# Kernel tuning notes

Measured on AMD Instinct MI355X. Metric: run time of the kernel, lower is better.

Reference implementation:

```python
import jax, jax.numpy as jnp
import numpy as np

R, C, N, E, H, F, ED, G, L = 1, 4, 50000, 200000, 128, 128, 16, 64, 2


def setup_inputs() -> dict:
    key = jax.random.key(0)
    ks = jax.random.split(key, 16)
    s = 0.05
    return {
        "x": jax.random.normal(ks[0], (R * C * N, H), jnp.float32),
        "batch": jnp.sort(jax.random.randint(ks[1], (N,), 0, G)),
        "edge_index": jax.random.randint(ks[2], (2, E), 0, N),
        "edge_attr": jax.random.normal(ks[3], (1, 1, E, ED), jnp.float32),
        "node_mask": jax.random.uniform(ks[4], (R, C, N, 1), jnp.float32),
        "edge_mask": jax.random.uniform(ks[5], (R, C, E, 1), jnp.float32),
        "W_be": jax.random.normal(ks[6], (ED, H), jnp.float32) * s,
        "b_be": jnp.zeros((H,), jnp.float32),
        "eps": jnp.zeros((L,), jnp.float32),
        "W1": jax.random.normal(ks[7], (L, H, H), jnp.float32) * s,
        "b1": jnp.zeros((L, H), jnp.float32),
        "W2": jax.random.normal(ks[8], (L, H, H), jnp.float32) * s,
        "b2": jnp.zeros((L, H), jnp.float32),
        "Wm1": jax.random.normal(ks[9], (H, H), jnp.float32) * s,
        "bm1": jnp.zeros((H,), jnp.float32),
        "Wm2": jax.random.normal(ks[10], (H, F), jnp.float32) * s,
        "bm2": jnp.zeros((F,), jnp.float32),
    }


def reference(x, batch, edge_index, edge_attr, node_mask, edge_mask,
              W_be, b_be, eps, W1, b1, W2, b2, Wm1, bm1, Wm2, bm2):
    gelu = lambda v: jax.nn.gelu(v, approximate=False)  # torch F.gelu default is erf
    src, dst = edge_index[0], edge_index[1]
    # bond encoder, shared across conv layers: (1,1,E,H)
    ee = edge_attr @ W_be + b_be
    for l in range(L):
        ux = x.reshape(R, C, N, H)
        # gather + add + GELU + edge-weight multiply: (R,C,E,H)
        msg = gelu(ux[:, :, src, :] + ee) * edge_mask
        # scatter_sum over edges into destination nodes
        agg = jnp.zeros_like(ux).at[:, :, dst, :].add(msg)
        h = (1.0 + eps[l]) * x + agg.reshape(x.shape)
        # conv MLP: Linear -> GELU -> Linear, then outer GELU (norm=Identity, dropout=0)
        h = gelu(h @ W1[l] + b1[l]) @ W2[l] + b2[l]
        x = gelu(h)
    # final node MLP (PyG MLP, norm=None): Linear -> GELU -> Linear
    x = gelu(x @ Wm1 + bm1) @ Wm2 + bm2  # (R*C*N, F)
    x4 = x.reshape(R, C, N, F)
    # masked mean-pool per (repeat, centroid, graph)
    num = jnp.zeros((R, C, G, F), x.dtype).at[:, :, batch, :].add(x4 * node_mask)
    den = jnp.zeros((R, C, G, 1), x.dtype).at[:, :, batch, :].add(node_mask) + 1e-7
    pooled = (num / den).transpose(0, 2, 1, 3).reshape(-1, F)  # (R*G*C, F)
    return pooled
```

## Files before the change

### kernel.cpp

```cpp
#include <hip/hip_runtime.h>
#include <math.h>

#define NN 50000
#define EN 200000
#define CC 4
#define HH 128
#define GG 64
#define LDSA 136
#define LDSF 132

typedef __attribute__((ext_vector_type(8))) short bs8;
typedef __attribute__((ext_vector_type(4))) float f32x4;
typedef __attribute__((ext_vector_type(2))) float f32x2;

__device__ __forceinline__ unsigned short f2bf(float f) {
  unsigned int u = __float_as_uint(f);
  u += 0x7FFFu + ((u >> 16) & 1u);
  return (unsigned short)(u >> 16);
}
__device__ __forceinline__ float bf2f(unsigned short h) {
  return __uint_as_float(((unsigned int)h) << 16);
}
__device__ __forceinline__ float gelu_f(float x) {
  float z = fabsf(x) * 0.7071067811865476f;
  float t = __builtin_amdgcn_rcpf(fmaf(0.3275911f, z, 1.0f));
  float poly = t * fmaf(t, fmaf(t, fmaf(t, fmaf(t, 1.061405429f, -1.453152027f),
                                        1.421413741f), -0.284496736f), 0.254829592f);
  float e = fmaf(-poly, __expf(-z * z), 1.0f);
  return 0.5f * x * (1.0f + copysignf(e, x));
}
__device__ __forceinline__ float gelu2_f(float x) {
  float z = fabsf(x) * 0.7071067811865476f;
  float t = __builtin_amdgcn_rcpf(fmaf(0.3275911f, z, 1.0f));
  float poly = t * fmaf(t, fmaf(t, fmaf(t, fmaf(t, 1.061405429f, -1.453152027f),
                                        1.421413741f), -0.284496736f), 0.254829592f);
  float e = fmaf(-poly, __expf(-z * z), 1.0f);
  return x * (1.0f + copysignf(e, x));
}

__global__ __launch_bounds__(256) void count_kernel(const int* __restrict__ dst,
                                                    int* __restrict__ counts) {
  int e = blockIdx.x * 256 + threadIdx.x;
  if (e < EN) atomicAdd(&counts[dst[e]], 1);
}

__global__ __launch_bounds__(256) void block_sum_kernel(const int* __restrict__ counts,
                                                        int* __restrict__ bsums) {
  int tid = threadIdx.x;
  int i = blockIdx.x * 256 + tid;
  int v = (i < NN) ? counts[i] : 0;
#pragma unroll
  for (int d = 1; d < 64; d <<= 1) v += __shfl_xor(v, d);
  __shared__ int ws4[4];
  if ((tid & 63) == 0) ws4[tid >> 6] = v;
  __syncthreads();
  if (tid == 0) bsums[blockIdx.x] = ws4[0] + ws4[1] + ws4[2] + ws4[3];
}

__global__ __launch_bounds__(256) void bsum_scan_kernel(const int* __restrict__ bsums,
                                                        int* __restrict__ boffs, int nb) {
  int tid = threadIdx.x, lane = tid & 63, wv = tid >> 6;
  int v = (tid < nb) ? bsums[tid] : 0;
  int s = v;
#pragma unroll
  for (int d = 1; d < 64; d <<= 1) { int t = __shfl_up(s, d); if (lane >= d) s += t; }
  __shared__ int wsum[4];
  if (lane == 63) wsum[wv] = s;
  __syncthreads();
  int pre = 0;
  for (int j = 0; j < wv; ++j) pre += wsum[j];
  if (tid < nb) boffs[tid] = pre + s - v;
}

__global__ __launch_bounds__(256) void block_scan_kernel(const int* __restrict__ counts,
// ... 41 lines not shown
                                                     unsigned short* __restrict__ wts) {
  int m = blockIdx.x >> 6;
  int idx = (blockIdx.x & 63) * 256 + threadIdx.x;
  const float* src = (m == 0) ? W1 : (m == 1) ? W1 + 16384 : (m == 2) ? W2
                     : (m == 3) ? W2 + 16384 : (m == 4) ? Wm1 : Wm2;
  unsigned short* dhi = wts + m * 32768;
  unsigned short* dlo = dhi + 16384;
  int n = idx >> 7, k = idx & 127;
  float v = src[k * HH + n];
  unsigned short hi = f2bf(v);
  dhi[n * HH + k] = hi;
  dlo[n * HH + k] = f2bf(v - bf2f(hi));
}

__global__ __launch_bounds__(256) void ee_kernel(const float* __restrict__ eattr,
                                                 const float* __restrict__ Wbe,
                                                 const float* __restrict__ bbe,
                                                 float* __restrict__ ee) {
  __shared__ float Ws[16 * HH];
  __shared__ float Ea[16 * 16];
  int tid = threadIdx.x;
  int e0 = blockIdx.x * 16;
#pragma unroll
  for (int i = 0; i < 8; ++i) Ws[tid + i * 256] = Wbe[tid + i * 256];
  Ea[tid] = eattr[(size_t)e0 * 16 + tid];
  __syncthreads();
  int h = tid & 127, half = tid >> 7;
  float bb = bbe[h];
#pragma unroll
  for (int j = 0; j < 8; ++j) {
    int el = j * 2 + half;
    float acc = bb;
#pragma unroll
    for (int d = 0; d < 16; ++d) acc += Ea[el * 16 + d] * Ws[d * HH + h];
    ee[(size_t)(e0 + el) * HH + h] = acc;
  }
}

__global__ __launch_bounds__(256) void agg_kernel(const float* __restrict__ x,
                                                  const float* __restrict__ ee,
                                                  const int* __restrict__ off,
                                                  const int2* __restrict__ csr_es,
                                                  const float4* __restrict__ emask_s,
                                                  const float* __restrict__ epsp, int layer,
                                                  float* __restrict__ hout) {
  int wv = threadIdx.x >> 6, lane = threadIdx.x & 63;
  int v = blockIdx.x * 4 + wv;
  int c2 = lane * 2;
  float2 acc[CC];
#pragma unroll
  for (int c = 0; c < CC; ++c) { acc[c].x = 0.f; acc[c].y = 0.f; }
  int beg = off[v], end = off[v + 1];

  float2 eeC; float2 xC[CC]; float emC[CC];
  int2 esN = make_int2(0, 0);
  eeC.x = 0.f; eeC.y = 0.f;
#pragma unroll
  for (int c = 0; c < CC; ++c) { xC[c].x = 0.f; xC[c].y = 0.f; emC[c] = 0.f; }

  if (beg < end) {
    int2 es0 = csr_es[beg];
    eeC = *(const float2*)(ee + (size_t)es0.x * HH + c2);
#pragma unroll
    for (int c = 0; c < CC; ++c)
      xC[c] = *(const float2*)(x + ((size_t)c * NN + es0.y) * HH + c2);
    float4 m = emask_s[beg];
    emC[0] = 0.5f * m.x; emC[1] = 0.5f * m.y; emC[2] = 0.5f * m.z; emC[3] = 0.5f * m.w;
    if (beg + 1 < end) esN = csr_es[beg + 1];
  }

  for (int t = beg; t < end; ++t) {
    float2 eeB; float2 xB[CC]; float emB[CC];
    int2 esNN = make_int2(0, 0);
    if (t + 1 < end) {
      eeB = *(const float2*)(ee + (size_t)esN.x * HH + c2);
#pragma unroll
      for (int c = 0; c < CC; ++c)
        xB[c] = *(const float2*)(x + ((size_t)c * NN + esN.y) * HH + c2);
      float4 m = emask_s[t + 1];
      emB[0] = 0.5f * m.x; emB[1] = 0.5f * m.y; emB[2] = 0.5f * m.z; emB[3] = 0.5f * m.w;
      if (t + 2 < end) esNN = csr_es[t + 2];
    } else {
      eeB.x = 0.f; eeB.y = 0.f;
#pragma unroll
      for (int c = 0; c < CC; ++c) { xB[c].x = 0.f; xB[c].y = 0.f; emB[c] = 0.f; }
    }
#pragma unroll
    for (int c = 0; c < CC; ++c) {
      acc[c].x += gelu2_f(xC[c].x + eeC.x) * emC[c];
      acc[c].y += gelu2_f(xC[c].y + eeC.y) * emC[c];
    }
    eeC = eeB;
#pragma unroll
    for (int c = 0; c < CC; ++c) { xC[c] = xB[c]; emC[c] = emB[c]; }
    esN = esNN;
  }

  float ep = 1.0f + epsp[layer];
#pragma unroll
  for (int c = 0; c < CC; ++c) {
    float2 xs = *(const float2*)(x + ((size_t)c * NN + v) * HH + c2);
    f32x2 o;
    o[0] = fmaf(ep, xs.x, acc[c].x);
    o[1] = fmaf(ep, xs.y, acc[c].y);
    __builtin_nontemporal_store(o, (f32x2*)(hout + ((size_t)c * NN + v) * HH + c2));
  }
}

__global__ __launch_bounds__(256, 2) void mlp_kernel(
    const float* __restrict__ in,
    const unsigned short* __restrict__ w1hi, const unsigned short* __restrict__ w1lo,
    const float* __restrict__ b1,
    const unsigned short* __restrict__ w2hi, const unsigned short* __restrict__ w2lo,
    const float* __restrict__ b2,
    float* __restrict__ out) {
  __shared__ __align__(16) unsigned short AB[2 * 64 * HH];
  unsigned short* Ahi = AB;
  unsigned short* Alo = AB + 64 * HH;
  int tid = threadIdx.x;
  int row0 = blockIdx.x * 64;
  int lane = tid & 63, wq = tid >> 6;
  int ln = lane & 15, quad = lane >> 4;

  bs8 b1h[4][2], b1l[4][2];
#pragma unroll
  for (int ks = 0; ks < 4; ++ks)
#pragma unroll
    for (int nt = 0; nt < 2; ++nt) {
      int wrow = ((wq * 2 + nt) * 16 + ln) * HH + ks * 32 + quad * 8;
      b1h[ks][nt] = *(const bs8*)(w1hi + wrow);
      b1l[ks][nt] = *(const bs8*)(w1lo + wrow);
    }

#pragma unroll
  for (int i = 0; i < 4; ++i) {
    int idx = tid + i * 256;
    int r = idx >> 4, blk = idx & 15;
    const float* p = in + (size_t)(row0 + r) * HH + blk * 8;
    f32x4 v0 = __builtin_nontemporal_load((const f32x4*)p);
    f32x4 v1 = __builtin_nontemporal_load((const f32x4*)(p + 4));
    bs8 h, l;
    h[0] = f2bf(v0[0]); h[1] = f2bf(v0[1]); h[2] = f2bf(v0[2]); h[3] = f2bf(v0[3]);
    h[4] = f2bf(v1[0]); h[5] = f2bf(v1[1]); h[6] = f2bf(v1[2]); h[7] = f2bf(v1[3]);
    l[0] = f2bf(v0[0] - bf2f(h[0])); l[1] = f2bf(v0[1] - bf2f(h[1]));
    l[2] = f2bf(v0[2] - bf2f(h[2])); l[3] = f2bf(v0[3] - bf2f(h[3]));
    l[4] = f2bf(v1[0] - bf2f(h[4])); l[5] = f2bf(v1[1] - bf2f(h[5]));
    l[6] = f2bf(v1[2] - bf2f(h[6])); l[7] = f2bf(v1[3] - bf2f(h[7]));
    int sb = blk ^ (r & 15);
    *(bs8*)(Ahi + r * HH + sb * 8) = h;
    *(bs8*)(Alo + r * HH + sb * 8) = l;
  }
  __syncthreads();

  f32x4 acc[4][2];
#pragma unroll
  for (int mt = 0; mt < 4; ++mt)
#pragma unroll
    for (int nt = 0; nt < 2; ++nt)
#pragma unroll
      for (int r = 0; r < 4; ++r) acc[mt][nt][r] = 0.f;
#pragma unroll
  for (int ks = 0; ks < 4; ++ks) {
    bs8 ah[4], al[4];
    int sb = ((ks * 4 + quad) ^ ln) * 8;
#pragma unroll
    for (int mt = 0; mt < 4; ++mt) {
      ah[mt] = *(const bs8*)(Ahi + (mt * 16 + ln) * HH + sb);
      al[mt] = *(const bs8*)(Alo + (mt * 16 + ln) * HH + sb);
    }
#pragma unroll
    for (int nt = 0; nt < 2; ++nt)
#pragma unroll
      for (int mt = 0; mt < 4; ++mt) {
        acc[mt][nt] = __builtin_amdgcn_mfma_f32_16x16x32_bf16(al[mt], b1h[ks][nt], acc[mt][nt], 0, 0, 0);
        acc[mt][nt] = __builtin_amdgcn_mfma_f32_16x16x32_bf16(ah[mt], b1l[ks][nt], acc[mt][nt], 0, 0, 0);
        acc[mt][nt] = __builtin_amdgcn_mfma_f32_16x16x32_bf16(ah[mt], b1h[ks][nt], acc[mt][nt], 0, 0, 0);
      }
  }
  __syncthreads();

  bs8 b2h[4][2], b2l[4][2];
#pragma unroll
  for (int ks = 0; ks < 4; ++ks)
#pragma unroll
    for (int nt = 0; nt < 2; ++nt) {
      int wrow = ((wq * 2 + nt) * 16 + ln) * HH + ks * 32 + quad * 8;
      b2h[ks][nt] = *(const bs8*)(w2hi + wrow);
      b2l[ks][nt] = *(const bs8*)(w2lo + wrow);
    }

#pragma unroll
  for (int nt = 0; nt < 2; ++nt) {
    int col = (wq * 2 + nt) * 16 + ln;
    int cb = col >> 3, co = col & 7;
    float bb = b1[col];
#pragma unroll
    for (int mt = 0; mt < 4; ++mt)
#pragma unroll
      for (int r = 0; r < 4; ++r) {
        float tv = gelu_f(acc[mt][nt][r] + bb);
        unsigned short th = f2bf(tv);
        int rr = mt * 16 + quad * 4 + r;
        int sof = rr * HH + (cb ^ (rr & 15)) * 8 + co;
        Ahi[sof] = th;
        Alo[sof] = f2bf(tv - bf2f(th));
      }
  }
  __syncthreads();

#pragma unroll
  for (int mt = 0; mt < 4; ++mt)
#pragma unroll
    for (int nt = 0; nt < 2; ++nt)
#pragma unroll
      for (int r = 0; r < 4; ++r) acc[mt][nt][r] = 0.f;
#pragma unroll
  for (int ks = 0; ks < 4; ++ks) {
    bs8 ah[4], al[4];
    int sb = ((ks * 4 + quad) ^ ln) * 8;
#pragma unroll
    for (int mt = 0; mt < 4; ++mt) {
      ah[mt] = *(const bs8*)(Ahi + (mt * 16 + ln) * HH + sb);
      al[mt] = *(const bs8*)(Alo + (mt * 16 + ln) * HH + sb);
    }
#pragma unroll
    for (int nt = 0; nt < 2; ++nt)
#pragma unroll
      for (int mt = 0; mt < 4; ++mt) {
        acc[mt][nt] = __builtin_amdgcn_mfma_f32_16x16x32_bf16(al[mt], b2h[ks][nt], acc[mt][nt], 0, 0, 0);
        acc[mt][nt] = __builtin_amdgcn_mfma_f32_16x16x32_bf16(ah[mt], b2l[ks][nt], acc[mt][nt], 0, 0, 0);
        acc[mt][nt] = __builtin_amdgcn_mfma_f32_16x16x32_bf16(ah[mt], b2h[ks][nt], acc[mt][nt], 0, 0, 0);
      }
  }
#pragma unroll
  for (int nt = 0; nt < 2; ++nt) {
    int col = (wq * 2 + nt) * 16 + ln;
    float bb = b2[col];
#pragma unroll
    for (int mt = 0; mt < 4; ++mt)
#pragma unroll
      for (int r = 0; r < 4; ++r) {
        float o = gelu_f(acc[mt][nt][r] + bb);
        out[(size_t)(row0 + mt * 16 + quad * 4 + r) * HH + col] = o;
      }
  }
}

__global__ __launch_bounds__(256, 2) void mlp_pool_kernel(
    const float* __restrict__ in,
    const unsigned short* __restrict__ w1hi, const unsigned short* __restrict__ w1lo,
    const float* __restrict__ b1,
    const unsigned short* __restrict__ w2hi, const unsigned short* __restrict__ w2lo,
    const float* __restrict__ b2,
    const float* __restrict__ nmask, const int* __restrict__ batch,
    float* __restrict__ num) {
  __shared__ __align__(16) unsigned short AB[128 * LDSA];
  __shared__ int kk[64];
  unsigned short* Ahi = AB;
  unsigned short* Alo = AB + 64 * LDSA;
  int tid = threadIdx.x;
  int row0 = blockIdx.x * 64;
  int lane = tid & 63, wq = tid >> 6;
  int ln = lane & 15, quad = lane >> 4;

  bs8 b1h[4][2], b1l[4][2];
#pragma unroll
  for (int ks = 0; ks < 4; ++ks)
#pragma unroll
    for (int nt = 0; nt < 2; ++nt) {
      int wrow = ((wq * 2 + nt) * 16 + ln) * HH + ks * 32 + quad * 8;
      b1h[ks][nt] = *(const bs8*)(w1hi + wrow);
      b1l[ks][nt] = *(const bs8*)(w1lo + wrow);
    }
#pragma unroll
  for (int i = 0; i < 8; ++i) {
    int idx = tid + i * 256;
    int r = idx >> 5, cc4 = idx & 31;
    f32x4 vv = __builtin_nontemporal_load(
        (const f32x4*)(in + (size_t)(row0 + r) * HH + cc4 * 4));
    unsigned short h0 = f2bf(vv[0]), h1 = f2bf(vv[1]), h2 = f2bf(vv[2]), h3 = f2bf(vv[3]);
    ushort4 hv; hv.x = h0; hv.y = h1; hv.z = h2; hv.w = h3;
    ushort4 lv;
    lv.x = f2bf(vv[0] - bf2f(h0)); lv.y = f2bf(vv[1] - bf2f(h1));
    lv.z = f2bf(vv[2] - bf2f(h2)); lv.w = f2bf(vv[3] - bf2f(h3));
    *(ushort4*)(Ahi + r * LDSA + cc4 * 4) = hv;
    *(ushort4*)(Alo + r * LDSA + cc4 * 4) = lv;
  }
  if (tid < 64) {
    int gr = row0 + tid;
    int c = gr / NN;
    int n = gr - c * NN;
    kk[tid] = (c << 6) | batch[n];
  }
  __syncthreads();

  f32x4 acc[4][2];
#pragma unroll
  for (int mt = 0; mt < 4; ++mt)
#pragma unroll
    for (int nt = 0; nt < 2; ++nt)
#pragma unroll
      for (int r = 0; r < 4; ++r) acc[mt][nt][r] = 0.f;
#pragma unroll
  for (int ks = 0; ks < 4; ++ks) {
    bs8 ah[4], al[4];
#pragma unroll
    for (int mt = 0; mt < 4; ++mt) {
      ah[mt] = *(const bs8*)(Ahi + (mt * 16 + ln) * LDSA + ks * 32 + quad * 8);
      al[mt] = *(const bs8*)(Alo + (mt * 16 + ln) * LDSA + ks * 32 + quad * 8);
    }
#pragma unroll
    for (int nt = 0; nt < 2; ++nt)
#pragma unroll
      for (int mt = 0; mt < 4; ++mt) {
        acc[mt][nt] = __builtin_amdgcn_mfma_f32_16x16x32_bf16(al[mt], b1h[ks][nt], acc[mt][nt], 0, 0, 0);
        acc[mt][nt] = __builtin_amdgcn_mfma_f32_16x16x32_bf16(ah[mt], b1l[ks][nt], acc[mt][nt], 0, 0, 0);
        acc[mt][nt] = __builtin_amdgcn_mfma_f32_16x16x32_bf16(ah[mt], b1h[ks][nt], acc[mt][nt], 0, 0, 0);
      }
  }
  __syncthreads();

  bs8 b2h[4][2], b2l[4][2];
#pragma unroll
  for (int ks = 0; ks < 4; ++ks)
#pragma unroll
    for (int nt = 0; nt < 2; ++nt) {
      int wrow = ((wq * 2 + nt) * 16 + ln) * HH + ks * 32 + quad * 8;
      b2h[ks][nt] = *(const bs8*)(w2hi + wrow);
      b2l[ks][nt] = *(const bs8*)(w2lo + wrow);
    }
#pragma unroll
  for (int nt = 0; nt < 2; ++nt) {
    int col = (wq * 2 + nt) * 16 + ln;
    float bb = b1[col];
#pragma unroll
    for (int mt = 0; mt < 4; ++mt)
#pragma unroll
      for (int r = 0; r < 4; ++r) {
        float tv = gelu_f(acc[mt][nt][r] + bb);
        unsigned short th = f2bf(tv);
        int rr = mt * 16 + quad * 4 + r;
        Ahi[rr * LDSA + col] = th;
        Alo[rr * LDSA + col] = f2bf(tv - bf2f(th));
      }
  }
  __syncthreads();

#pragma unroll
  for (int mt = 0; mt < 4; ++mt)
#pragma unroll
    for (int nt = 0; nt < 2; ++nt)
#pragma unroll
      for (int r = 0; r < 4; ++r) acc[mt][nt][r] = 0.f;
#pragma unroll
  for (int ks = 0; ks < 4; ++ks) {
    bs8 ah[4], al[4];
#pragma unroll
    for (int mt = 0; mt < 4; ++mt) {
      ah[mt] = *(const bs8*)(Ahi + (mt * 16 + ln) * LDSA + ks * 32 + quad * 8);
      al[mt] = *(const bs8*)(Alo + (mt * 16 + ln) * LDSA + ks * 32 + quad * 8);
    }
#pragma unroll
    for (int nt = 0; nt < 2; ++nt)
#pragma unroll
      for (int mt = 0; mt < 4; ++mt) {
        acc[mt][nt] = __builtin_amdgcn_mfma_f32_16x16x32_bf16(al[mt], b2h[ks][nt], acc[mt][nt], 0, 0, 0);
        acc[mt][nt] = __builtin_amdgcn_mfma_f32_16x16x32_bf16(ah[mt], b2l[ks][nt], acc[mt][nt], 0, 0, 0);
        acc[mt][nt] = __builtin_amdgcn_mfma_f32_16x16x32_bf16(ah[mt], b2h[ks][nt], acc[mt][nt], 0, 0, 0);
      }
  }
  __syncthreads();
  float* Tf = (float*)AB;
#pragma unroll
  for (int nt = 0; nt < 2; ++nt) {
    int col = (wq * 2 + nt) * 16 + ln;
    float bb = b2[col];
#pragma unroll
    for (int mt = 0; mt < 4; ++mt)
#pragma unroll
      for (int r = 0; r < 4; ++r) {
        int rl = mt * 16 + quad * 4 + r;
        int gr = row0 + rl;
        Tf[rl * LDSF + col] = (acc[mt][nt][r] + bb) * nmask[gr];
      }
  }
  __syncthreads();
  if (tid < 128) {
    int col = tid;
    float a2 = 0.f;
    int cur = kk[0];
    for (int r = 0; r < 64; ++r) {
      int k2 = kk[r];
      if (k2 != cur) {
        atomicAdd(&num[((size_t)(cur & 63) * CC + (cur >> 6)) * HH + col], a2);
        a2 = 0.f;
        cur = k2;
      }
      a2 += Tf[r * LDSF + col];
    }
    atomicAdd(&num[((size_t)(cur & 63) * CC + (cur >> 6)) * HH + col], a2);
  }
}

__global__ __launch_bounds__(256) void pool_finalize_kernel(const float* __restrict__ num,
                                                            const int* __restrict__ batch,
                                                            const float* __restrict__ nmask,
                                                            float* __restrict__ outp) {
  int g = blockIdx.x >> 2, c = blockIdx.x & 3;
  int lo = 0, hi = NN;
  while (lo < hi) { int m = (lo + hi) >> 1; if (batch[m] < g) lo = m + 1; else hi = m; }
  int start = lo;
  hi = NN;
  while (lo < hi) { int m = (lo + hi) >> 1; if (batch[m] < g + 1) lo = m + 1; else hi = m; }
  int end = lo;
  int tid = threadIdx.x;
  float d = 0.f;
  for (int n = start + tid; n < end; n += 256) d += nmask[c * NN + n];
#pragma unroll
  for (int k = 1; k < 64; k <<= 1) d += __shfl_xor(d, k);
  __shared__ float ws4[4];
  if ((tid & 63) == 0) ws4[tid >> 6] = d;
// ... 8 lines not shown
extern "C" void kernel_launch(void* const* d_in, const int* in_sizes, int n_in,
                              void* d_out, int out_size, void* d_ws, size_t ws_size,
                              hipStream_t stream) {
  const float* x_in  = (const float*)d_in[0];
  const int*   batch = (const int*)d_in[1];
  const int*   eidx  = (const int*)d_in[2];
  const float* eattr = (const float*)d_in[3];
  const float* nmask = (const float*)d_in[4];
  const float* emask = (const float*)d_in[5];
  const float* Wbe   = (const float*)d_in[6];
  const float* bbe   = (const float*)d_in[7];
  const float* epsp  = (const float*)d_in[8];
  const float* W1    = (const float*)d_in[9];
  const float* b1    = (const float*)d_in[10];
  const float* W2    = (const float*)d_in[11];
  const float* b2    = (const float*)d_in[12];
  const float* Wm1   = (const float*)d_in[13];
  const float* bm1   = (const float*)d_in[14];
  const float* Wm2   = (const float*)d_in[15];
  const float* bm2   = (const float*)d_in[16];
  float* outp = (float*)d_out;

  const int* srcp = eidx;
  const int* dstp = eidx + EN;

  char* ws = (char*)d_ws;
  float* ee   = (float*)(ws);
  float* hbuf = (float*)(ws + 102400000);
  float* xbuf = (float*)(ws + 204800000);
  int* counts  = (int*)(ws + 307200000);
  int* offsets = (int*)(ws + 307400000);
  int* cursor  = (int*)(ws + 307600008);
  int2* csr_es = (int2*)(ws + 307800016);
  float4* emask_s = (float4*)(ws + 309400016);
  unsigned short* wts = (unsigned short*)(ws + 312600016);
  int* bsums = (int*)ws;
  int* boffs = (int*)(ws + 1024);
  float* num = (float*)ws;

  const int NB = (NN + 255) / 256;

  hipMemsetAsync(counts, 0, NN * sizeof(int), stream);
  count_kernel<<<(EN + 255) / 256, 256, 0, stream>>>(dstp, counts);
  block_sum_kernel<<<NB, 256, 0, stream>>>(counts, bsums);
  bsum_scan_kernel<<<1, 256, 0, stream>>>(bsums, boffs, NB);
  block_scan_kernel<<<NB, 256, 0, stream>>>(counts, boffs, offsets, cursor);
  fill_kernel<<<(EN + 255) / 256, 256, 0, stream>>>(dstp, srcp, emask, cursor, csr_es, emask_s);

  prep_w_kernel<<<384, 256, 0, stream>>>(W1, W2, Wm1, Wm2, wts);

  ee_kernel<<<EN / 16, 256, 0, stream>>>(eattr, Wbe, bbe, ee);

  agg_kernel<<<NN / 4, 256, 0, stream>>>(x_in, ee, offsets, csr_es, emask_s, epsp, 0, hbuf);
  mlp_kernel<<<(CC * NN) / 64, 256, 0, stream>>>(hbuf, wts + 0, wts + 16384, b1,
                                                 wts + 65536, wts + 81920, b2, xbuf);
  agg_kernel<<<NN / 4, 256, 0, stream>>>(xbuf, ee, offsets, csr_es, emask_s, epsp, 1, hbuf);
  mlp_kernel<<<(CC * NN) / 64, 256, 0, stream>>>(hbuf, wts + 32768, wts + 49152, b1 + 128,
                                                 wts + 98304, wts + 114688, b2 + 128, xbuf);
  hipMemsetAsync(num, 0, 131072, stream);
  mlp_pool_kernel<<<(CC * NN) / 64, 256, 0, stream>>>(xbuf, wts + 131072, wts + 147456, bm1,
                                                      wts + 163840, wts + 180224, bm2,
                                                      nmask, batch, num);
  pool_finalize_kernel<<<GG * CC, 256, 0, stream>>>(num, batch, nmask, outp);
}
```

Before: 717.2 us.

## Load MLP input fragments directly from global and stream weights per k-step

The first GEMM of both MLP kernels now loads its A fragments straight from global memory into registers, converting to bf16 hi/lo there instead of staging through LDS, and drops one barrier. Weight fragments are loaded per k-step instead of being held for all k-steps, and launch bounds rise from 2 to 4 blocks per CU. The aim is to cut register pressure and LDS traffic so occupancy goes up and latency is hidden better. In exchange, every wave now reads the same input rows from global memory, giving 4x redundant (mostly cached) loads and weight reloads inside the k loop.

```diff
diff --git a/kernel.cpp b/kernel.cpp
--- a/kernel.cpp
+++ b/kernel.cpp
@@ -20,6 +20,14 @@
 }
 __device__ __forceinline__ float bf2f(unsigned short h) {
   return __uint_as_float(((unsigned int)h) << 16);
+}
+__device__ __forceinline__ void cvt_hi_lo(const f32x4& v0, const f32x4& v1, bs8& h, bs8& l) {
+  h[0] = f2bf(v0[0]); h[1] = f2bf(v0[1]); h[2] = f2bf(v0[2]); h[3] = f2bf(v0[3]);
+  h[4] = f2bf(v1[0]); h[5] = f2bf(v1[1]); h[6] = f2bf(v1[2]); h[7] = f2bf(v1[3]);
+  l[0] = f2bf(v0[0] - bf2f(h[0])); l[1] = f2bf(v0[1] - bf2f(h[1]));
+  l[2] = f2bf(v0[2] - bf2f(h[2])); l[3] = f2bf(v0[3] - bf2f(h[3]));
+  l[4] = f2bf(v1[0] - bf2f(h[4])); l[5] = f2bf(v1[1] - bf2f(h[5]));
+  l[6] = f2bf(v1[2] - bf2f(h[6])); l[7] = f2bf(v1[3] - bf2f(h[7]));
 }
 __device__ __forceinline__ float gelu_f(float x) {
   float z = fabsf(x) * 0.7071067811865476f;
@@ -222,7 +230,7 @@
   }
 }
 
-__global__ __launch_bounds__(256, 2) void mlp_kernel(
+__global__ __launch_bounds__(256, 4) void mlp_kernel(
     const float* __restrict__ in,
     const unsigned short* __restrict__ w1hi, const unsigned short* __restrict__ w1lo,
     const float* __restrict__ b1,
@@ -237,72 +245,38 @@
   int lane = tid & 63, wq = tid >> 6;
   int ln = lane & 15, quad = lane >> 4;
 
-  bs8 b1h[4][2], b1l[4][2];
-#pragma unroll
-  for (int ks = 0; ks < 4; ++ks)
+  f32x4 acc[4][2];
+#pragma unroll
+  for (int mt = 0; mt < 4; ++mt)
+#pragma unroll
+    for (int nt = 0; nt < 2; ++nt)
+#pragma unroll
+      for (int r = 0; r < 4; ++r) acc[mt][nt][r] = 0.f;
+
+#pragma unroll
+  for (int ks = 0; ks < 4; ++ks) {
+    bs8 bh[2], bl[2];
 #pragma unroll
     for (int nt = 0; nt < 2; ++nt) {
       int wrow = ((wq * 2 + nt) * 16 + ln) * HH + ks * 32 + quad * 8;
-      b1h[ks][nt] = *(const bs8*)(w1hi + wrow);
-      b1l[ks][nt] = *(const bs8*)(w1lo + wrow);
-    }
-
-#pragma unroll
-  for (int i = 0; i < 4; ++i) {
-    int idx = tid + i * 256;
-    int r = idx >> 4, blk = idx & 15;
-    const float* p = in + (size_t)(row0 + r) * HH + blk * 8;
-    f32x4 v0 = __builtin_nontemporal_load((const f32x4*)p);
-    f32x4 v1 = __builtin_nontemporal_load((const f32x4*)(p + 4));
-    bs8 h, l;
-    h[0] = f2bf(v0[0]); h[1] = f2bf(v0[1]); h[2] = f2bf(v0[2]); h[3] = f2bf(v0[3]);
-    h[4] = f2bf(v1[0]); h[5] = f2bf(v1[1]); h[6] = f2bf(v1[2]); h[7] = f2bf(v1[3]);
-    l[0] = f2bf(v0[0] - bf2f(h[0])); l[1] = f2bf(v0[1] - bf2f(h[1]));
-    l[2] = f2bf(v0[2] - bf2f(h[2])); l[3] = f2bf(v0[3] - bf2f(h[3]));
-    l[4] = f2bf(v1[0] - bf2f(h[4])); l[5] = f2bf(v1[1] - bf2f(h[5]));
-    l[6] = f2bf(v1[2] - bf2f(h[6])); l[7] = f2bf(v1[3] - bf2f(h[7]));
-    int sb = blk ^ (r & 15);
-    *(bs8*)(Ahi + r * HH + sb * 8) = h;
-    *(bs8*)(Alo + r * HH + sb * 8) = l;
-  }
-  __syncthreads();
-
-  f32x4 acc[4][2];
-#pragma unroll
-  for (int mt = 0; mt < 4; ++mt)
-#pragma unroll
-    for (int nt = 0; nt < 2; ++nt)
-#pragma unroll
-      for (int r = 0; r < 4; ++r) acc[mt][nt][r] = 0.f;
-#pragma unroll
-  for (int ks = 0; ks < 4; ++ks) {
-    bs8 ah[4], al[4];
-    int sb = ((ks * 4 + quad) ^ ln) * 8;
+      bh[nt] = *(const bs8*)(w1hi + wrow);
+      bl[nt] = *(const bs8*)(w1lo + wrow);
+    }
 #pragma unroll
     for (int mt = 0; mt < 4; ++mt) {
-      ah[mt] = *(const bs8*)(Ahi + (mt * 16 + ln) * HH + sb);
-      al[mt] = *(const bs8*)(Alo + (mt * 16 + ln) * HH + sb);
-    }
-#pragma unroll
-    for (int nt = 0; nt < 2; ++nt)
-#pragma unroll
-      for (int mt = 0; mt < 4; ++mt) {
-        acc[mt][nt] = __builtin_amdgcn_mfma_f32_16x16x32_bf16(al[mt], b1h[ks][nt], acc[mt][nt], 0, 0, 0);
-        acc[mt][nt] = __builtin_amdgcn_mfma_f32_16x16x32_bf16(ah[mt], b1l[ks][nt], acc[mt][nt], 0, 0, 0);
-        acc[mt][nt] = __builtin_amdgcn_mfma_f32_16x16x32_bf16(ah[mt], b1h[ks][nt], acc[mt][nt], 0, 0, 0);
-      }
-  }
-  __syncthreads();
-
-  bs8 b2h[4][2], b2l[4][2];
-#pragma unroll
-  for (int ks = 0; ks < 4; ++ks)
-#pragma unroll
-    for (int nt = 0; nt < 2; ++nt) {
-      int wrow = ((wq * 2 + nt) * 16 + ln) * HH + ks * 32 + quad * 8;
-      b2h[ks][nt] = *(const bs8*)(w2hi + wrow);
-      b2l[ks][nt] = *(const bs8*)(w2lo + wrow);
-    }
+      const float* p = in + (size_t)(row0 + mt * 16 + ln) * HH + ks * 32 + quad * 8;
+      f32x4 v0 = __builtin_nontemporal_load((const f32x4*)p);
+      f32x4 v1 = __builtin_nontemporal_load((const f32x4*)(p + 4));
+      bs8 ah, al;
+      cvt_hi_lo(v0, v1, ah, al);
+#pragma unroll
+      for (int nt = 0; nt < 2; ++nt) {
+        acc[mt][nt] = __builtin_amdgcn_mfma_f32_16x16x32_bf16(al, bh[nt], acc[mt][nt], 0, 0, 0);
+        acc[mt][nt] = __builtin_amdgcn_mfma_f32_16x16x32_bf16(ah, bl[nt], acc[mt][nt], 0, 0, 0);
+        acc[mt][nt] = __builtin_amdgcn_mfma_f32_16x16x32_bf16(ah, bh[nt], acc[mt][nt], 0, 0, 0);
+      }
+    }
+  }
 
 #pragma unroll
   for (int nt = 0; nt < 2; ++nt) {
@@ -331,6 +305,13 @@
       for (int r = 0; r < 4; ++r) acc[mt][nt][r] = 0.f;
 #pragma unroll
   for (int ks = 0; ks < 4; ++ks) {
+    bs8 bh[2], bl[2];
+#pragma unroll
+    for (int nt = 0; nt < 2; ++nt) {
+      int wrow = ((wq * 2 + nt) * 16 + ln) * HH + ks * 32 + quad * 8;
+      bh[nt] = *(const bs8*)(w2hi + wrow);
+      bl[nt] = *(const bs8*)(w2lo + wrow);
+    }
     bs8 ah[4], al[4];
     int sb = ((ks * 4 + quad) ^ ln) * 8;
 #pragma unroll
@@ -339,12 +320,12 @@
       al[mt] = *(const bs8*)(Alo + (mt * 16 + ln) * HH + sb);
     }
 #pragma unroll
-    for (int nt = 0; nt < 2; ++nt)
-#pragma unroll
-      for (int mt = 0; mt < 4; ++mt) {
-        acc[mt][nt] = __builtin_amdgcn_mfma_f32_16x16x32_bf16(al[mt], b2h[ks][nt], acc[mt][nt], 0, 0, 0);
-        acc[mt][nt] = __builtin_amdgcn_mfma_f32_16x16x32_bf16(ah[mt], b2l[ks][nt], acc[mt][nt], 0, 0, 0);
-        acc[mt][nt] = __builtin_amdgcn_mfma_f32_16x16x32_bf16(ah[mt], b2h[ks][nt], acc[mt][nt], 0, 0, 0);
+    for (int mt = 0; mt < 4; ++mt)
+#pragma unroll
+      for (int nt = 0; nt < 2; ++nt) {
+        acc[mt][nt] = __builtin_amdgcn_mfma_f32_16x16x32_bf16(al[mt], bh[nt], acc[mt][nt], 0, 0, 0);
+        acc[mt][nt] = __builtin_amdgcn_mfma_f32_16x16x32_bf16(ah[mt], bl[nt], acc[mt][nt], 0, 0, 0);
+        acc[mt][nt] = __builtin_amdgcn_mfma_f32_16x16x32_bf16(ah[mt], bh[nt], acc[mt][nt], 0, 0, 0);
       }
   }
 #pragma unroll
@@ -361,7 +342,7 @@
   }
 }
 
-__global__ __launch_bounds__(256, 2) void mlp_pool_kernel(
+__global__ __launch_bounds__(256, 4) void mlp_pool_kernel(
     const float* __restrict__ in,
     const unsigned short* __restrict__ w1hi, const unsigned short* __restrict__ w1lo,
     const float* __restrict__ b1,
@@ -378,36 +359,12 @@
   int lane = tid & 63, wq = tid >> 6;
   int ln = lane & 15, quad = lane >> 4;
 
-  bs8 b1h[4][2], b1l[4][2];
-#pragma unroll
-  for (int ks = 0; ks < 4; ++ks)
-#pragma unroll
-    for (int nt = 0; nt < 2; ++nt) {
-      int wrow = ((wq * 2 + nt) * 16 + ln) * HH + ks * 32 + quad * 8;
-      b1h[ks][nt] = *(const bs8*)(w1hi + wrow);
-      b1l[ks][nt] = *(const bs8*)(w1lo + wrow);
-    }
-#pragma unroll
-  for (int i = 0; i < 8; ++i) {
-    int idx = tid + i * 256;
-    int r = idx >> 5, cc4 = idx & 31;
-    f32x4 vv = __builtin_nontemporal_load(
-        (const f32x4*)(in + (size_t)(row0 + r) * HH + cc4 * 4));
-    unsigned short h0 = f2bf(vv[0]), h1 = f2bf(vv[1]), h2 = f2bf(vv[2]), h3 = f2bf(vv[3]);
-    ushort4 hv; hv.x = h0; hv.y = h1; hv.z = h2; hv.w = h3;
-    ushort4 lv;
-    lv.x = f2bf(vv[0] - bf2f(h0)); lv.y = f2bf(vv[1] - bf2f(h1));
-    lv.z = f2bf(vv[2] - bf2f(h2)); lv.w = f2bf(vv[3] - bf2f(h3));
-    *(ushort4*)(Ahi + r * LDSA + cc4 * 4) = hv;
-    *(ushort4*)(Alo + r * LDSA + cc4 * 4) = lv;
-  }
   if (tid < 64) {
     int gr = row0 + tid;
     int c = gr / NN;
     int n = gr - c * NN;
     kk[tid] = (c << 6) | batch[n];
   }
-  __syncthreads();
 
   f32x4 acc[4][2];
 #pragma unroll
@@ -416,34 +373,32 @@
     for (int nt = 0; nt < 2; ++nt)
 #pragma unroll
       for (int r = 0; r < 4; ++r) acc[mt][nt][r] = 0.f;
+
 #pragma unroll
   for (int ks = 0; ks < 4; ++ks) {
-    bs8 ah[4], al[4];
-#pragma unroll
-    for (int mt = 0; mt < 4; ++mt) {
-      ah[mt] = *(const bs8*)(Ahi + (mt * 16 + ln) * LDSA + ks * 32 + quad * 8);
-      al[mt] = *(const bs8*)(Alo + (mt * 16 + ln) * LDSA + ks * 32 + quad * 8);
-    }
-#pragma unroll
-    for (int nt = 0; nt < 2; ++nt)
-#pragma unroll
-      for (int mt = 0; mt < 4; ++mt) {
-        acc[mt][nt] = __builtin_amdgcn_mfma_f32_16x16x32_bf16(al[mt], b1h[ks][nt], acc[mt][nt], 0, 0, 0);
-        acc[mt][nt] = __builtin_amdgcn_mfma_f32_16x16x32_bf16(ah[mt], b1l[ks][nt], acc[mt][nt], 0, 0, 0);
-        acc[mt][nt] = __builtin_amdgcn_mfma_f32_16x16x32_bf16(ah[mt], b1h[ks][nt], acc[mt][nt], 0, 0, 0);
-      }
-  }
-  __syncthreads();
-
-  bs8 b2h[4][2], b2l[4][2];
-#pragma unroll
-  for (int ks = 0; ks < 4; ++ks)
+    bs8 bh[2], bl[2];
 #pragma unroll
     for (int nt = 0; nt < 2; ++nt) {
       int wrow = ((wq * 2 + nt) * 16 + ln) * HH + ks * 32 + quad * 8;
-      b2h[ks][nt] = *(const bs8*)(w2hi + wrow);
-      b2l[ks][nt] = *(const bs8*)(w2lo + wrow);
-    }
+      bh[nt] = *(const bs8*)(w1hi + wrow);
+      bl[nt] = *(const bs8*)(w1lo + wrow);
+    }
+#pragma unroll
+    for (int mt = 0; mt < 4; ++mt) {
+      const float* p = in + (size_t)(row0 + mt * 16 + ln) * HH + ks * 32 + quad * 8;
+      f32x4 v0 = __builtin_nontemporal_load((const f32x4*)p);
+      f32x4 v1 = __builtin_nontemporal_load((const f32x4*)(p + 4));
+      bs8 ah, al;
+      cvt_hi_lo(v0, v1, ah, al);
+#pragma unroll
+      for (int nt = 0; nt < 2; ++nt) {
+        acc[mt][nt] = __builtin_amdgcn_mfma_f32_16x16x32_bf16(al, bh[nt], acc[mt][nt], 0, 0, 0);
+        acc[mt][nt] = __builtin_amdgcn_mfma_f32_16x16x32_bf16(ah, bl[nt], acc[mt][nt], 0, 0, 0);
+        acc[mt][nt] = __builtin_amdgcn_mfma_f32_16x16x32_bf16(ah, bh[nt], acc[mt][nt], 0, 0, 0);
+      }
+    }
+  }
+
 #pragma unroll
   for (int nt = 0; nt < 2; ++nt) {
     int col = (wq * 2 + nt) * 16 + ln;
@@ -469,6 +424,13 @@
       for (int r = 0; r < 4; ++r) acc[mt][nt][r] = 0.f;
 #pragma unroll
   for (int ks = 0; ks < 4; ++ks) {
+    bs8 bh[2], bl[2];
+#pragma unroll
+    for (int nt = 0; nt < 2; ++nt) {
+      int wrow = ((wq * 2 + nt) * 16 + ln) * HH + ks * 32 + quad * 8;
+      bh[nt] = *(const bs8*)(w2hi + wrow);
+      bl[nt] = *(const bs8*)(w2lo + wrow);
+    }
     bs8 ah[4], al[4];
 #pragma unroll
     for (int mt = 0; mt < 4; ++mt) {
@@ -476,12 +438,12 @@
       al[mt] = *(const bs8*)(Alo + (mt * 16 + ln) * LDSA + ks * 32 + quad * 8);
     }
 #pragma unroll
-    for (int nt = 0; nt < 2; ++nt)
-#pragma unroll
-      for (int mt = 0; mt < 4; ++mt) {
-        acc[mt][nt] = __builtin_amdgcn_mfma_f32_16x16x32_bf16(al[mt], b2h[ks][nt], acc[mt][nt], 0, 0, 0);
-        acc[mt][nt] = __builtin_amdgcn_mfma_f32_16x16x32_bf16(ah[mt], b2l[ks][nt], acc[mt][nt], 0, 0, 0);
-        acc[mt][nt] = __builtin_amdgcn_mfma_f32_16x16x32_bf16(ah[mt], b2h[ks][nt], acc[mt][nt], 0, 0, 0);
+    for (int mt = 0; mt < 4; ++mt)
+#pragma unroll
+      for (int nt = 0; nt < 2; ++nt) {
+        acc[mt][nt] = __builtin_amdgcn_mfma_f32_16x16x32_bf16(al[mt], bh[nt], acc[mt][nt], 0, 0, 0);
+        acc[mt][nt] = __builtin_amdgcn_mfma_f32_16x16x32_bf16(ah[mt], bl[nt], acc[mt][nt], 0, 0, 0);
+        acc[mt][nt] = __builtin_amdgcn_mfma_f32_16x16x32_bf16(ah[mt], bh[nt], acc[mt][nt], 0, 0, 0);
       }
   }
   __syncthreads();
```

New measurement: 864.5 us. 1.21x slower.

## Process two row tiles per MLP block with input prefetch; deepen agg gather pipeline

Applied to the files above, without the earlier changes.

The layer MLP kernel now handles two 64-row tiles per block, launching half as many blocks, and loads the second tile's input rows into registers while the first tile's GEMMs run, so global load latency is hidden behind MFMA work. The aggregation kernel's software pipeline is deepened from one edge ahead to two edges ahead, giving the gathered x and edge-embedding loads more time to land. The MLP code is also factored into helper functions. The cost is higher register pressure from the prefetched tile and extra pipeline registers, which could reduce occupancy. The half-size grid may also leave compute units less evenly loaded.

```diff
diff --git a/kernel.cpp b/kernel.cpp
--- a/kernel.cpp
+++ b/kernel.cpp
@@ -8,6 +8,8 @@
 #define GG 64
 #define LDSA 136
 #define LDSF 132
+#define NTILE 3125
+#define HTILE 1563
 
 typedef __attribute__((ext_vector_type(8))) short bs8;
 typedef __attribute__((ext_vector_type(4))) float f32x4;
@@ -20,6 +22,14 @@
 }
 __device__ __forceinline__ float bf2f(unsigned short h) {
   return __uint_as_float(((unsigned int)h) << 16);
+}
+__device__ __forceinline__ void cvt_hi_lo(const f32x4& v0, const f32x4& v1, bs8& h, bs8& l) {
+  h[0] = f2bf(v0[0]); h[1] = f2bf(v0[1]); h[2] = f2bf(v0[2]); h[3] = f2bf(v0[3]);
+  h[4] = f2bf(v1[0]); h[5] = f2bf(v1[1]); h[6] = f2bf(v1[2]); h[7] = f2bf(v1[3]);
+  l[0] = f2bf(v0[0] - bf2f(h[0])); l[1] = f2bf(v0[1] - bf2f(h[1]));
+  l[2] = f2bf(v0[2] - bf2f(h[2])); l[3] = f2bf(v0[3] - bf2f(h[3]));
+  l[4] = f2bf(v1[0] - bf2f(h[4])); l[5] = f2bf(v1[1] - bf2f(h[5]));
+  l[6] = f2bf(v1[2] - bf2f(h[6])); l[7] = f2bf(v1[3] - bf2f(h[7]));
 }
 __device__ __forceinline__ float gelu_f(float x) {
   float z = fabsf(x) * 0.7071067811865476f;
@@ -167,48 +177,67 @@
   for (int c = 0; c < CC; ++c) { acc[c].x = 0.f; acc[c].y = 0.f; }
   int beg = off[v], end = off[v + 1];
 
-  float2 eeC; float2 xC[CC]; float emC[CC];
-  int2 esN = make_int2(0, 0);
-  eeC.x = 0.f; eeC.y = 0.f;
-#pragma unroll
-  for (int c = 0; c < CC; ++c) { xC[c].x = 0.f; xC[c].y = 0.f; emC[c] = 0.f; }
+  float2 eeC, eeB;
+  float2 xC[CC], xB[CC];
+  float emC[CC], emB[CC];
+  int2 es2 = make_int2(0, 0), es3 = make_int2(0, 0);
+  eeC.x = eeC.y = eeB.x = eeB.y = 0.f;
+#pragma unroll
+  for (int c = 0; c < CC; ++c) {
+    xC[c].x = xC[c].y = xB[c].x = xB[c].y = 0.f;
+    emC[c] = emB[c] = 0.f;
+  }
 
   if (beg < end) {
-    int2 es0 = csr_es[beg];
-    eeC = *(const float2*)(ee + (size_t)es0.x * HH + c2);
+    int2 e0 = csr_es[beg];
+    eeC = *(const float2*)(ee + (size_t)e0.x * HH + c2);
 #pragma unroll
     for (int c = 0; c < CC; ++c)
-      xC[c] = *(const float2*)(x + ((size_t)c * NN + es0.y) * HH + c2);
+      xC[c] = *(const float2*)(x + ((size_t)c * NN + e0.y) * HH + c2);
     float4 m = emask_s[beg];
     emC[0] = 0.5f * m.x; emC[1] = 0.5f * m.y; emC[2] = 0.5f * m.z; emC[3] = 0.5f * m.w;
-    if (beg + 1 < end) esN = csr_es[beg + 1];
-  }
+  }
+  if (beg + 1 < end) {
+    int2 e1 = csr_es[beg + 1];
+    eeB = *(const float2*)(ee + (size_t)e1.x * HH + c2);
+#pragma unroll
+    for (int c = 0; c < CC; ++c)
+      xB[c] = *(const float2*)(x + ((size_t)c * NN + e1.y) * HH + c2);
+    float4 m = emask_s[beg + 1];
+    emB[0] = 0.5f * m.x; emB[1] = 0.5f * m.y; emB[2] = 0.5f * m.z; emB[3] = 0.5f * m.w;
+  }
+  if (beg + 2 < end) es2 = csr_es[beg + 2];
 
   for (int t = beg; t < end; ++t) {
-    float2 eeB; float2 xB[CC]; float emB[CC];
-    int2 esNN = make_int2(0, 0);
-    if (t + 1 < end) {
-      eeB = *(const float2*)(ee + (size_t)esN.x * HH + c2);
+    float2 eeD;
+    float2 xD[CC];
+    float emD[CC];
+    if (t + 2 < end) {
+      eeD = *(const float2*)(ee + (size_t)es2.x * HH + c2);
 #pragma unroll
       for (int c = 0; c < CC; ++c)
-        xB[c] = *(const float2*)(x + ((size_t)c * NN + esN.y) * HH + c2);
-      float4 m = emask_s[t + 1];
-      emB[0] = 0.5f * m.x; emB[1] = 0.5f * m.y; emB[2] = 0.5f * m.z; emB[3] = 0.5f * m.w;
-      if (t + 2 < end) esNN = csr_es[t + 2];
+        xD[c] = *(const float2*)(x + ((size_t)c * NN + es2.y) * HH + c2);
+      float4 m = emask_s[t + 2];
+      emD[0] = 0.5f * m.x; emD[1] = 0.5f * m.y; emD[2] = 0.5f * m.z; emD[3] = 0.5f * m.w;
+      es3 = (t + 3 < end) ? csr_es[t + 3] : make_int2(0, 0);
     } else {
-      eeB.x = 0.f; eeB.y = 0.f;
-#pragma unroll
-      for (int c = 0; c < CC; ++c) { xB[c].x = 0.f; xB[c].y = 0.f; emB[c] = 0.f; }
+      eeD.x = eeD.y = 0.f;
+#pragma unroll
+      for (int c = 0; c < CC; ++c) { xD[c].x = xD[c].y = 0.f; emD[c] = 0.f; }
+      es3 = make_int2(0, 0);
     }
 #pragma unroll
     for (int c = 0; c < CC; ++c) {
       acc[c].x += gelu2_f(xC[c].x + eeC.x) * emC[c];
       acc[c].y += gelu2_f(xC[c].y + eeC.y) * emC[c];
     }
-    eeC = eeB;
-#pragma unroll
-    for (int c = 0; c < CC; ++c) { xC[c] = xB[c]; emC[c] = emB[c]; }
-    esN = esNN;
+    eeC = eeB; eeB = eeD;
+#pragma unroll
+    for (int c = 0; c < CC; ++c) {
+      xC[c] = xB[c]; xB[c] = xD[c];
+      emC[c] = emB[c]; emB[c] = emD[c];
+    }
+    es2 = es3;
   }
 
   float ep = 1.0f + epsp[layer];
@@ -219,6 +248,86 @@
     o[0] = fmaf(ep, xs.x, acc[c].x);
     o[1] = fmaf(ep, xs.y, acc[c].y);
     __builtin_nontemporal_store(o, (f32x2*)(hout + ((size_t)c * NN + v) * HH + c2));
+  }
+}
+
+__device__ __forceinline__ void loadW(const unsigned short* __restrict__ whi,
+                                      const unsigned short* __restrict__ wlo,
+                                      bs8 (&bh)[4][2], bs8 (&bl)[4][2],
+                                      int ln, int quad, int wq) {
+#pragma unroll
+  for (int ks = 0; ks < 4; ++ks)
+#pragma unroll
+    for (int nt = 0; nt < 2; ++nt) {
+      int wrow = ((wq * 2 + nt) * 16 + ln) * HH + ks * 32 + quad * 8;
+      bh[ks][nt] = *(const bs8*)(whi + wrow);
+      bl[ks][nt] = *(const bs8*)(wlo + wrow);
+    }
+}
+__device__ __forceinline__ void zacc(f32x4 (&acc)[4][2]) {
+#pragma unroll
+  for (int mt = 0; mt < 4; ++mt)
+#pragma unroll
+    for (int nt = 0; nt < 2; ++nt)
+#pragma unroll
+      for (int r = 0; r < 4; ++r) acc[mt][nt][r] = 0.f;
+}
+__device__ __forceinline__ void gemm3(const unsigned short* Ahi, const unsigned short* Alo,
+                                      const bs8 (&bh)[4][2], const bs8 (&bl)[4][2],
+                                      f32x4 (&acc)[4][2], int ln, int quad) {
+#pragma unroll
+  for (int ks = 0; ks < 4; ++ks) {
+    bs8 ah[4], al[4];
+    int sb = ((ks * 4 + quad) ^ ln) * 8;
+#pragma unroll
+    for (int mt = 0; mt < 4; ++mt) {
+      ah[mt] = *(const bs8*)(Ahi + (mt * 16 + ln) * HH + sb);
+      al[mt] = *(const bs8*)(Alo + (mt * 16 + ln) * HH + sb);
+    }
+#pragma unroll
+    for (int nt = 0; nt < 2; ++nt)
+#pragma unroll
+      for (int mt = 0; mt < 4; ++mt) {
+        acc[mt][nt] = __builtin_amdgcn_mfma_f32_16x16x32_bf16(al[mt], bh[ks][nt], acc[mt][nt], 0, 0, 0);
+        acc[mt][nt] = __builtin_amdgcn_mfma_f32_16x16x32_bf16(ah[mt], bl[ks][nt], acc[mt][nt], 0, 0, 0);
+        acc[mt][nt] = __builtin_amdgcn_mfma_f32_16x16x32_bf16(ah[mt], bh[ks][nt], acc[mt][nt], 0, 0, 0);
+      }
+  }
+}
+__device__ __forceinline__ void tstage(unsigned short* Ahi, unsigned short* Alo,
+                                       const float* __restrict__ b1v, f32x4 (&acc)[4][2],
+                                       int ln, int quad, int wq) {
+#pragma unroll
+  for (int nt = 0; nt < 2; ++nt) {
+    int col = (wq * 2 + nt) * 16 + ln;
+    int cb = col >> 3, co = col & 7;
+    float bb = b1v[col];
+#pragma unroll
+    for (int mt = 0; mt < 4; ++mt)
+#pragma unroll
+      for (int r = 0; r < 4; ++r) {
+        float tv = gelu_f(acc[mt][nt][r] + bb);
+        unsigned short th = f2bf(tv);
+        int rr = mt * 16 + quad * 4 + r;
+        int sof = rr * HH + (cb ^ (rr & 15)) * 8 + co;
+        Ahi[sof] = th;
+        Alo[sof] = f2bf(tv - bf2f(th));
+      }
+  }
+}
+__device__ __forceinline__ void epilog(float* __restrict__ out, const float* __restrict__ b2v,
+                                       f32x4 (&acc)[4][2], int row0, int ln, int quad, int wq) {
+#pragma unroll
+  for (int nt = 0; nt < 2; ++nt) {
+    int col = (wq * 2 + nt) * 16 + ln;
+    float bb = b2v[col];
+#pragma unroll
+    for (int mt = 0; mt < 4; ++mt)
+#pragma unroll
+      for (int r = 0; r < 4; ++r) {
+        float o = gelu_f(acc[mt][nt][r] + bb);
+        out[(size_t)(row0 + mt * 16 + quad * 4 + r) * HH + col] = o;
+      }
   }
 }
 
@@ -233,20 +342,15 @@
   unsigned short* Ahi = AB;
   unsigned short* Alo = AB + 64 * HH;
   int tid = threadIdx.x;
-  int row0 = blockIdx.x * 64;
   int lane = tid & 63, wq = tid >> 6;
   int ln = lane & 15, quad = lane >> 4;
-
-  bs8 b1h[4][2], b1l[4][2];
-#pragma unroll
-  for (int ks = 0; ks < 4; ++ks)
-#pragma unroll
-    for (int nt = 0; nt < 2; ++nt) {
-      int wrow = ((wq * 2 + nt) * 16 + ln) * HH + ks * 32 + quad * 8;
-      b1h[ks][nt] = *(const bs8*)(w1hi + wrow);
-      b1l[ks][nt] = *(const bs8*)(w1lo + wrow);
-    }
-
+  int t1 = blockIdx.x + HTILE;
+  bool has2 = (t1 < NTILE);
+  int row0 = blockIdx.x * 64;
+  int row1 = t1 * 64;
+
+  bs8 w1h[4][2], w1l[4][2];
+  loadW(w1hi, w1lo, w1h, w1l, ln, quad, wq);
 #pragma unroll
   for (int i = 0; i < 4; ++i) {
     int idx = tid + i * 256;
@@ -255,110 +359,65 @@
     f32x4 v0 = __builtin_nontemporal_load((const f32x4*)p);
     f32x4 v1 = __builtin_nontemporal_load((const f32x4*)(p + 4));
     bs8 h, l;
-    h[0] = f2bf(v0[0]); h[1] = f2bf(v0[1]); h[2] = f2bf(v0[2]); h[3] = f2bf(v0[3]);
-    h[4] = f2bf(v1[0]); h[5] = f2bf(v1[1]); h[6] = f2bf(v1[2]); h[7] = f2bf(v1[3]);
-    l[0] = f2bf(v0[0] - bf2f(h[0])); l[1] = f2bf(v0[1] - bf2f(h[1]));
-    l[2] = f2bf(v0[2] - bf2f(h[2])); l[3] = f2bf(v0[3] - bf2f(h[3]));
-    l[4] = f2bf(v1[0] - bf2f(h[4])); l[5] = f2bf(v1[1] - bf2f(h[5]));
-    l[6] = f2bf(v1[2] - bf2f(h[6])); l[7] = f2bf(v1[3] - bf2f(h[7]));
+    cvt_hi_lo(v0, v1, h, l);
     int sb = blk ^ (r & 15);
     *(bs8*)(Ahi + r * HH + sb * 8) = h;
     *(bs8*)(Alo + r * HH + sb * 8) = l;
   }
   __syncthreads();
 
+  f32x4 pa[4], pb[4];
+  if (has2) {
+#pragma unroll
+    for (int i = 0; i < 4; ++i) {
+      int idx = tid + i * 256;
+      int r = idx >> 4, blk = idx & 15;
+      const float* p = in + (size_t)(row1 + r) * HH + blk * 8;
+      pa[i] = __builtin_nontemporal_load((const f32x4*)p);
+      pb[i] = __builtin_nontemporal_load((const f32x4*)(p + 4));
+    }
+  }
+
   f32x4 acc[4][2];
-#pragma unroll
-  for (int mt = 0; mt < 4; ++mt)
-#pragma unroll
-    for (int nt = 0; nt < 2; ++nt)
-#pragma unroll
-      for (int r = 0; r < 4; ++r) acc[mt][nt][r] = 0.f;
-#pragma unroll
-  for (int ks = 0; ks < 4; ++ks) {
-    bs8 ah[4], al[4];
-    int sb = ((ks * 4 + quad) ^ ln) * 8;
-#pragma unroll
-    for (int mt = 0; mt < 4; ++mt) {
-      ah[mt] = *(const bs8*)(Ahi + (mt * 16 + ln) * HH + sb);
-      al[mt] = *(const bs8*)(Alo + (mt * 16 + ln) * HH + sb);
-    }
-#pragma unroll
-    for (int nt = 0; nt < 2; ++nt)
-#pragma unroll
-      for (int mt = 0; mt < 4; ++mt) {
-        acc[mt][nt] = __builtin_amdgcn_mfma_f32_16x16x32_bf16(al[mt], b1h[ks][nt], acc[mt][nt], 0, 0, 0);
-        acc[mt][nt] = __builtin_amdgcn_mfma_f32_16x16x32_bf16(ah[mt], b1l[ks][nt], acc[mt][nt], 0, 0, 0);
-        acc[mt][nt] = __builtin_amdgcn_mfma_f32_16x16x32_bf16(ah[mt], b1h[ks][nt], acc[mt][nt], 0, 0, 0);
-      }
-  }
-  __syncthreads();
-
-  bs8 b2h[4][2], b2l[4][2];
-#pragma unroll
-  for (int ks = 0; ks < 4; ++ks)
-#pragma unroll
-    for (int nt = 0; nt < 2; ++nt) {
-      int wrow = ((wq * 2 + nt) * 16 + ln) * HH + ks * 32 + quad * 8;
-      b2h[ks][nt] = *(const bs8*)(w2hi + wrow);
-      b2l[ks][nt] = *(const bs8*)(w2lo + wrow);
-    }
-
-#pragma unroll
-  for (int nt = 0; nt < 2; ++nt) {
-    int col = (wq * 2 + nt) * 16 + ln;
-    int cb = col >> 3, co = col & 7;
-    float bb = b1[col];
-#pragma unroll
-    for (int mt = 0; mt < 4; ++mt)
-#pragma unroll
-      for (int r = 0; r < 4; ++r) {
-        float tv = gelu_f(acc[mt][nt][r] + bb);
-        unsigned short th = f2bf(tv);
-        int rr = mt * 16 + quad * 4 + r;
-        int sof = rr * HH + (cb ^ (rr & 15)) * 8 + co;
-        Ahi[sof] = th;
-        Alo[sof] = f2bf(tv - bf2f(th));
-      }
-  }
-  __syncthreads();
-
-#pragma unroll
-  for (int mt = 0; mt < 4; ++mt)
-#pragma unroll
-    for (int nt = 0; nt < 2; ++nt)
-#pragma unroll
-      for (int r = 0; r < 4; ++r) acc[mt][nt][r] = 0.f;
-#pragma unroll
-  for (int ks = 0; ks < 4; ++ks) {
-    bs8 ah[4], al[4];
-    int sb = ((ks * 4 + quad) ^ ln) * 8;
-#pragma unroll
-    for (int mt = 0; mt < 4; ++mt) {
-      ah[mt] = *(const bs8*)(Ahi + (mt * 16 + ln) * HH + sb);
-      al[mt] = *(const bs8*)(Alo + (mt * 16 + ln) * HH + sb);
-    }
-#pragma unroll
-    for (int nt = 0; nt < 2; ++nt)
-#pragma unroll
-      for (int mt = 0; mt < 4; ++mt) {
-        acc[mt][nt] = __builtin_amdgcn_mfma_f32_16x16x32_bf16(al[mt], b2h[ks][nt], acc[mt][nt], 0, 0, 0);
-        acc[mt][nt] = __builtin_amdgcn_mfma_f32_16x16x32_bf16(ah[mt], b2l[ks][nt], acc[mt][nt], 0, 0, 0);
-        acc[mt][nt] = __builtin_amdgcn_mfma_f32_16x16x32_bf16(ah[mt], b2h[ks][nt], acc[mt][nt], 0, 0, 0);
-      }
-  }
-#pragma unroll
-  for (int nt = 0; nt < 2; ++nt) {
-    int col = (wq * 2 + nt) * 16 + ln;
-    float bb = b2[col];
-#pragma unroll
-    for (int mt = 0; mt < 4; ++mt)
-#pragma unroll
-      for (int r = 0; r < 4; ++r) {
-        float o = gelu_f(acc[mt][nt][r] + bb);
-        out[(size_t)(row0 + mt * 16 + quad * 4 + r) * HH + col] = o;
-      }
-  }
+  zacc(acc);
+  gemm3(Ahi, Alo, w1h, w1l, acc, ln, quad);
+  __syncthreads();
+
+  bs8 w2h[4][2], w2l[4][2];
+  loadW(w2hi, w2lo, w2h, w2l, ln, quad, wq);
+  tstage(Ahi, Alo, b1, acc, ln, quad, wq);
+  __syncthreads();
+
+  zacc(acc);
+  gemm3(Ahi, Alo, w2h, w2l, acc, ln, quad);
+  epilog(out, b2, acc, row0, ln, quad, wq);
+
+  if (!has2) return;
+  __syncthreads();
+  loadW(w1hi, w1lo, w1h, w1l, ln, quad, wq);
+#pragma unroll
+  for (int i = 0; i < 4; ++i) {
+    int idx = tid + i * 256;
+    int r = idx >> 4, blk = idx & 15;
+    bs8 h, l;
+    cvt_hi_lo(pa[i], pb[i], h, l);
+    int sb = blk ^ (r & 15);
+    *(bs8*)(Ahi + r * HH + sb * 8) = h;
+    *(bs8*)(Alo + r * HH + sb * 8) = l;
+  }
+  __syncthreads();
+
+  zacc(acc);
+  gemm3(Ahi, Alo, w1h, w1l, acc, ln, quad);
+  __syncthreads();
+
+  loadW(w2hi, w2lo, w2h, w2l, ln, quad, wq);
+  tstage(Ahi, Alo, b1, acc, ln, quad, wq);
+  __syncthreads();
+
+  zacc(acc);
+  gemm3(Ahi, Alo, w2h, w2l, acc, ln, quad);
+  epilog(out, b2, acc, row1, ln, quad, wq);
 }
 
 __global__ __launch_bounds__(256, 2) void mlp_pool_kernel(
@@ -379,14 +438,7 @@
   int ln = lane & 15, quad = lane >> 4;
 
   bs8 b1h[4][2], b1l[4][2];
-#pragma unroll
-  for (int ks = 0; ks < 4; ++ks)
-#pragma unroll
-    for (int nt = 0; nt < 2; ++nt) {
-      int wrow = ((wq * 2 + nt) * 16 + ln) * HH + ks * 32 + quad * 8;
-      b1h[ks][nt] = *(const bs8*)(w1hi + wrow);
-      b1l[ks][nt] = *(const bs8*)(w1lo + wrow);
-    }
+  loadW(w1hi, w1lo, b1h, b1l, ln, quad, wq);
 #pragma unroll
   for (int i = 0; i < 8; ++i) {
     int idx = tid + i * 256;
@@ -410,12 +462,7 @@
   __syncthreads();
 
   f32x4 acc[4][2];
-#pragma unroll
-  for (int mt = 0; mt < 4; ++mt)
-#pragma unroll
-    for (int nt = 0; nt < 2; ++nt)
-#pragma unroll
-      for (int r = 0; r < 4; ++r) acc[mt][nt][r] = 0.f;
+  zacc(acc);
 #pragma unroll
   for (int ks = 0; ks < 4; ++ks) {
     bs8 ah[4], al[4];
@@ -436,14 +483,7 @@
   __syncthreads();
 
   bs8 b2h[4][2], b2l[4][2];
-#pragma unroll
-  for (int ks = 0; ks < 4; ++ks)
-#pragma unroll
-    for (int nt = 0; nt < 2; ++nt) {
-      int wrow = ((wq * 2 + nt) * 16 + ln) * HH + ks * 32 + quad * 8;
-      b2h[ks][nt] = *(const bs8*)(w2hi + wrow);
-      b2l[ks][nt] = *(const bs8*)(w2lo + wrow);
-    }
+  loadW(w2hi, w2lo, b2h, b2l, ln, quad, wq);
 #pragma unroll
   for (int nt = 0; nt < 2; ++nt) {
     int col = (wq * 2 + nt) * 16 + ln;
@@ -461,12 +501,7 @@
   }
   __syncthreads();
 
-#pragma unroll
-  for (int mt = 0; mt < 4; ++mt)
-#pragma unroll
-    for (int nt = 0; nt < 2; ++nt)
-#pragma unroll
-      for (int r = 0; r < 4; ++r) acc[mt][nt][r] = 0.f;
+  zacc(acc);
 #pragma unroll
   for (int ks = 0; ks < 4; ++ks) {
     bs8 ah[4], al[4];
@@ -596,14 +631,14 @@
   ee_kernel<<<EN / 16, 256, 0, stream>>>(eattr, Wbe, bbe, ee);
 
   agg_kernel<<<NN / 4, 256, 0, stream>>>(x_in, ee, offsets, csr_es, emask_s, epsp, 0, hbuf);
-  mlp_kernel<<<(CC * NN) / 64, 256, 0, stream>>>(hbuf, wts + 0, wts + 16384, b1,
-                                                 wts + 65536, wts + 81920, b2, xbuf);
+  mlp_kernel<<<HTILE, 256, 0, stream>>>(hbuf, wts + 0, wts + 16384, b1,
+                                        wts + 65536, wts + 81920, b2, xbuf);
   agg_kernel<<<NN / 4, 256, 0, stream>>>(xbuf, ee, offsets, csr_es, emask_s, epsp, 1, hbuf);
-  mlp_kernel<<<(CC * NN) / 64, 256, 0, stream>>>(hbuf, wts + 32768, wts + 49152, b1 + 128,
-                                                 wts + 98304, wts + 114688, b2 + 128, xbuf);
+  mlp_kernel<<<HTILE, 256, 0, stream>>>(hbuf, wts + 32768, wts + 49152, b1 + 128,
+                                        wts + 98304, wts + 114688, b2 + 128, xbuf);
   hipMemsetAsync(num, 0, 131072, stream);
-  mlp_pool_kernel<<<(CC * NN) / 64, 256, 0, stream>>>(xbuf, wts + 131072, wts + 147456, bm1,
-                                                      wts + 163840, wts + 180224, bm2,
-                                                      nmask, batch, num);
+  mlp_pool_kernel<<<NTILE, 256, 0, stream>>>(xbuf, wts + 131072, wts + 147456, bm1,
+                                             wts + 163840, wts + 180224, bm2,
+                                             nmask, batch, num);
   pool_finalize_kernel<<<GG * CC, 256, 0, stream>>>(num, batch, nmask, outp);
 }
```

New measurement: 743.0 us. +3.6%, slower.
